# Kernel optimization log

Hardware: AMD Instinct MI355X
Metric: run time of the kernel (lower is better)

## Reference

```python
import math
import jax, jax.numpy as jnp
import numpy as np
from jax import lax

W_DIM = 512
UP = 2
K = 3
LRELU_GAIN = math.sqrt(2.0)  # bias_act def_gain for 'lrelu'
CLAMP = 256.0                # conv_clamp * gain(=1)


def setup_inputs() -> dict:
    key = jax.random.key(0)
    ks = jax.random.split(key, 8)
    B, Cin, Cout, H = 16, 512, 512, 32
    return {
        "x": jax.random.normal(ks[0], (B, Cin, H, H), jnp.float32),
        "w_latent": jax.random.normal(ks[1], (B, W_DIM), jnp.float32),
        "affine_weight": jax.random.normal(ks[2], (Cin, W_DIM), jnp.float32),
        "affine_bias": jnp.ones((Cin,), jnp.float32),  # bias_init=1
        "conv_weight": jax.random.normal(ks[3], (Cout, Cin, K, K), jnp.float32),
        "noise": jax.random.normal(ks[4], (B, 1, 2 * H, 2 * H), jnp.float32),
        "noise_strength": jax.random.uniform(ks[5], (1,), jnp.float32),
        "bias": jax.random.normal(ks[6], (Cout,), jnp.float32),
    }


def reference(x, w_latent, affine_weight, affine_bias, conv_weight, noise, noise_strength, bias):
    B, Cin, H, W = x.shape
    Cout = conv_weight.shape[0]

    # EqualFullyConnectedLayer (linear act): style = w @ (W * 1/sqrt(in)).T + b
    style = w_latent @ (affine_weight * (1.0 / math.sqrt(W_DIM))).T + affine_bias  # [B, Cin]

    # Modulate + demodulate per-sample weights: [B, Cout, Cin, K, K]
    wmod = conv_weight[None] * style[:, None, :, None, None]
    dcoefs = lax.rsqrt(jnp.sum(wmod * wmod, axis=(2, 3, 4)) + 1e-8)  # [B, Cout]
    wmod = wmod * dcoefs[:, :, None, None, None]

    # Grouped transposed conv (stride=UP), batch-as-groups trick.
    # torch.conv_transpose2d(x, w.transpose, stride=UP) == dilated conv with
    # spatially-flipped modulated weight, lhs_dilation=UP, padding=K-1.
    w_eff = wmod.reshape(B * Cout, Cin, K, K)[:, :, ::-1, ::-1]
    x1 = x.reshape(1, B * Cin, H, W)
    y = lax.conv_general_dilated(
        x1, w_eff, window_strides=(1, 1),
        padding=[(K - 1, K - 1), (K - 1, K - 1)],
        lhs_dilation=(UP, UP), feature_group_count=B,
        dimension_numbers=("NCHW", "OIHW", "NCHW"))  # [1, B*Cout, 2H+1, 2W+1]

    # upfirdn2d: FIR low-pass (1,3,3,1) outer, normalized, gain=up^2, pad (1,1,1,1)
    f1 = jnp.array([1.0, 3.0, 3.0, 1.0], jnp.float32)
    f2 = jnp.outer(f1, f1)
    f2 = f2 / f2.sum() * (UP * UP)
    yc = y.reshape(B * Cout, 1, 2 * H + 1, 2 * W + 1)
    y = lax.conv_general_dilated(
        yc, f2[None, None], window_strides=(1, 1), padding=[(1, 1), (1, 1)],
        dimension_numbers=("NCHW", "OIHW", "NCHW"))
    y = y.reshape(B, Cout, 2 * H, 2 * W)

    # noise injection + fused bias + lrelu(gain=sqrt(2)) + clamp
    y = y + noise * noise_strength[0]
    y = y + bias[None, :, None, None]
    y = jax.nn.leaky_relu(y, negative_slope=0.2) * LRELU_GAIN
    return jnp.clip(y, -CLAMP, CLAMP)
```

## Files before the change

kernel.cpp:

```cpp
#include <hip/hip_runtime.h>
#include <hip/hip_bf16.h>


typedef unsigned short u16;
typedef unsigned int u32;
typedef u16 u16x8 __attribute__((ext_vector_type(8)));
typedef __bf16 bf16x8 __attribute__((ext_vector_type(8)));
typedef float f32x4 __attribute__((ext_vector_type(4)));

#define NB 16

__device__ __forceinline__ float bf2f(u16 v) {
  unsigned int u = ((unsigned int)v) << 16;
  float f;
  __builtin_memcpy(&f, &u, 4);
  return f;
}
__device__ __forceinline__ u16 f2bf(float f) {
  __hip_bfloat16 h = __float2bfloat16(f);
  u16 r;
  __builtin_memcpy(&r, &h, 2);
  return r;
}
__device__ __forceinline__ void async16(u16* lds, const u16* g) {
  __builtin_amdgcn_global_load_lds(
      (const __attribute__((address_space(1))) u32*)g,
      (__attribute__((address_space(3))) u32*)lds, 16, 0, 0);
}

__global__ __launch_bounds__(256) void k_style(const float* __restrict__ wl,
                                               const float* __restrict__ aw,
                                               const float* __restrict__ ab,
                                               float* __restrict__ style) {
  __shared__ float lw[512];
  const int b = blockIdx.y;
  const int c = blockIdx.x * 256 + threadIdx.x;
  for (int k = threadIdx.x; k < 512; k += 256) lw[k] = wl[b * 512 + k];
  __syncthreads();
  const float* row = aw + (size_t)c * 512;
  float acc = 0.f;
#pragma unroll 8
  for (int k = 0; k < 512; ++k) acc += lw[k] * row[k];
  style[b * 512 + c] = acc * 0.04419417382415922f + ab[c];
}

__global__ __launch_bounds__(256) void k_wprep(const float* __restrict__ cw,
                                               const float* __restrict__ style,
                                               float* __restrict__ dcoef,
                                               u16* __restrict__ W2) {
  __shared__ u16 lw[4608];
  __shared__ float wsq[512];
  const int o = blockIdx.x, t = threadIdx.x;
  const float* src = cw + (size_t)o * 4608;
  for (int v = t; v < 4608; v += 256) {
    unsigned c = (unsigned)v / 9u;
    unsigned kp = (unsigned)v % 9u;
    lw[kp * 512 + c] = f2bf(src[v]);
  }
  for (int c = t; c < 512; c += 256) {
    const float* p = src + (size_t)c * 9;
    float s = 0.f;
#pragma unroll
    for (int k = 0; k < 9; ++k) {
      float v = p[k];
      s += v * v;
    }
    wsq[c] = s;
  }
  __syncthreads();
  u16* dst = W2 + (size_t)o * 4608;
  for (int v = t; v < 576; v += 256)
    *(u16x8*)(dst + v * 8) = *(const u16x8*)(lw + v * 8);
  const int w = t >> 6, l = t & 63;
  for (int b = w; b < NB; b += 4) {
    float part = 0.f;
#pragma unroll
    for (int c = l; c < 512; c += 64) {
      float st = style[b * 512 + c];
      part += st * st * wsq[c];
    }
#pragma unroll
    for (int off = 32; off; off >>= 1) part += __shfl_down(part, off, 64);
    if (l == 0) dcoef[b * 512 + o] = 1.0f / sqrtf(part + 1e-8f);
  }
}

__global__ __launch_bounds__(256) void k_xt(const float* __restrict__ x,
                                            const float* __restrict__ style,
                                            u16* __restrict__ xT) {
  __shared__ u16 tile[64 * 66];
  const int b = blockIdx.z, c0 = blockIdx.y << 6, s0 = blockIdx.x << 6;
  const int t = threadIdx.x;
#pragma unroll
  for (int i = 0; i < 16; ++i) {
    int e = i * 256 + t;
    int cc = e >> 6, ss = e & 63;
    int c = c0 + cc;
    float v = x[(size_t)(b * 512 + c) * 1024 + s0 + ss] * style[b * 512 + c];
    tile[cc * 66 + ss] = f2bf(v);
  }
  __syncthreads();
#pragma unroll
  for (int e = 0; e < 2; ++e) {
    int idx = e * 256 + t;
    int sc = idx >> 3;
    int cg = (idx & 7) << 3;
    u16x8 v;
#pragma unroll
    for (int g = 0; g < 8; ++g) v[g] = tile[(cg + g) * 66 + sc];
    *(u16x8*)(xT + (size_t)(b * 1024 + s0 + sc) * 512 + c0 + cg) = v;
  }
}

__global__ __launch_bounds__(512, 2) void k_gemm(const u16* __restrict__ W2,
                                                 const u16* __restrict__ xT,
                                                 u16* __restrict__ Z) {
  __shared__ u16 At[4][8192];
  __shared__ u16 Bt[4][8192];
  const int t = threadIdx.x;
  const int m0 = blockIdx.y << 8;
  const int n0 = blockIdx.x << 8;
  const int l = t & 63;
  const int w = t >> 6;
  const int wm = w >> 2;
  const int wn = w & 3;
  const int lrow = l & 15;
  const int lk = l >> 4;

  const int sr = t >> 2;
  const int sch = ((t & 3) + (sr >> 1)) & 3;
  const u16* gA = W2 + (size_t)(m0 + sr) * 512 + (sch << 3);
  const u16* gB = xT + (size_t)(n0 + sr) * 512 + (sch << 3);
  const int wb = w << 9;

  const int sk8 = ((lk - (lrow >> 1)) & 3) << 3;
  const int arow = (wm << 7) + lrow;
  const int brow = (wn << 6) + lrow;

  f32x4 acc[8][4] = {};

#define STAGE_A(nb_, kt_)                                   \
  async16(&At[nb_][wb], gA + (kt_) * 32);                   \
  async16(&At[nb_][4096 + wb], gA + (kt_) * 32 + 65536)
#define STAGE_B(nb_, kt_)                                   \
  async16(&Bt[nb_][wb], gB + (kt_) * 32);                   \
  async16(&Bt[nb_][4096 + wb], gB + (kt_) * 32 + 65536)

  STAGE_A(0, 0);
  STAGE_B(0, 0);
  STAGE_A(1, 1);
  STAGE_B(1, 1);
  asm volatile("s_waitcnt vmcnt(4)" ::: "memory");
  asm volatile("s_barrier" ::: "memory");

  for (int kt = 0; kt < 16; ++kt) {
    const int buf = kt & 3;
    const int nb = (kt + 2) & 3;
    const u16* Ab = At[buf];
    const u16* Bb = Bt[buf];
    bf16x8 av[4], bv[4], av2[4];

#pragma unroll
    for (int i = 0; i < 4; ++i)
      av[i] = *(const bf16x8*)(Ab + (arow + i * 16) * 32 + sk8);
#pragma unroll
    for (int j = 0; j < 4; ++j)
      bv[j] = *(const bf16x8*)(Bb + (brow + j * 16) * 32 + sk8);
    if (kt < 14) { STAGE_A(nb, kt + 2); }
    asm volatile("s_barrier" ::: "memory");
    asm volatile("s_waitcnt lgkmcnt(0)" ::: "memory");
    __builtin_amdgcn_sched_barrier(0);
    __builtin_amdgcn_s_setprio(1);
#pragma unroll
    for (int i = 0; i < 4; ++i)
#pragma unroll
      for (int j = 0; j < 4; ++j)
        acc[i][j] = __builtin_amdgcn_mfma_f32_16x16x32_bf16(av[i], bv[j], acc[i][j], 0, 0, 0);
    __builtin_amdgcn_s_setprio(0);
    asm volatile("s_barrier" ::: "memory");

#pragma unroll
    for (int i = 0; i < 4; ++i)
      av2[i] = *(const bf16x8*)(Ab + (arow + 64 + i * 16) * 32 + sk8);
    if (kt < 14) { STAGE_B(nb, kt + 2); }
    asm volatile("s_barrier" ::: "memory");
    asm volatile("s_waitcnt lgkmcnt(0)" ::: "memory");
    __builtin_amdgcn_sched_barrier(0);
    __builtin_amdgcn_s_setprio(1);
#pragma unroll
    for (int i = 0; i < 4; ++i)
#pragma unroll
      for (int j = 0; j < 4; ++j)
        acc[i + 4][j] = __builtin_amdgcn_mfma_f32_16x16x32_bf16(av2[i], bv[j], acc[i + 4][j], 0, 0, 0);
    __builtin_amdgcn_s_setprio(0);

    if (kt < 14) {
      asm volatile("s_waitcnt vmcnt(4)" ::: "memory");
    } else if (kt == 14) {
      asm volatile("s_waitcnt vmcnt(0)" ::: "memory");
    }
    asm volatile("s_barrier" ::: "memory");
  }
#undef STAGE_A
#undef STAGE_B

  const int mr = m0 + (wm << 7) + (lk << 2);
  const int nc = n0 + (wn << 6) + lrow;
#pragma unroll
  for (int i = 0; i < 8; ++i)
#pragma unroll
    for (int j = 0; j < 4; ++j)
#pragma unroll
      for (int r = 0; r < 4; ++r)
        Z[(size_t)(mr + i * 16 + r) * 16384 + nc + j * 16] = f2bf(acc[i][j][r]);
}

__global__ __launch_bounds__(256) void k_scatter(
    const u16* __restrict__ Z, const float* __restrict__ dcoef,
    const float* __restrict__ noise, const float* __restrict__ nstr,
    const float* __restrict__ bias, float* __restrict__ out) {
  __shared__ u16 Zl[9 * 1024];
  __shared__ float Hl[3 * 2048];
  const int o = blockIdx.x;
  const int b = blockIdx.y;
  const int t = threadIdx.x;
  const u16* Zp = Z + (size_t)o * 9 * 16384 + (size_t)b * 1024;
  for (int v = t; v < 1152; v += 256) {
    int kp = v >> 7, off = (v & 127) << 3;
    *(u16x8*)(Zl + kp * 1024 + off) = *(const u16x8*)(Zp + (size_t)kp * 16384 + off);
  }
  __syncthreads();
#pragma unroll
  for (int e = 0; e < 12; ++e) {
    int idx = e * 256 + t;
    int ky = idx >> 10;
    int i = (idx >> 5) & 31;
    int j = idx & 31;
    const u16* P0 = Zl + (ky * 3 + 0) * 1024 + i * 32;
    const u16* P1 = P0 + 1024;
    const u16* P2 = P0 + 2048;
    float Ej = bf2f(P0[j]) + (j >= 1 ? bf2f(P2[j - 1]) : 0.f);
    float Ej1 = (j < 31 ? bf2f(P0[j + 1]) : 0.f) + bf2f(P2[j]);
    float Ojm = j >= 1 ? bf2f(P1[j - 1]) : 0.f;
    float Oj = bf2f(P1[j]);
    float Ojp = j < 31 ? bf2f(P1[j + 1]) : 0.f;
    float* hp = Hl + ky * 2048 + i * 64 + j;
    hp[0] = Ojm + 3.f * Ej + 3.f * Oj + Ej1;
    hp[32] = Ej + 3.f * Oj + 3.f * Ej1 + Ojp;
  }
  __syncthreads();
  const float dc = dcoef[b * 512 + o] * 0.0625f;
  const float ns = nstr[0];
  const float bo = bias[o];
  const int n = t & 63;
  const int i0 = (t >> 6) << 3;
  const int sw = ((n & 1) << 5) | (n >> 1);
  const float* H0 = Hl + sw;
  const float* H1 = Hl + 2048 + sw;
  const float* H2 = Hl + 4096 + sw;
  float h0 = H0[i0 * 64];
  float h1 = H1[i0 * 64];
  float h1p = (i0 > 0) ? H1[(i0 - 1) * 64] : 0.f;
  float h2p = (i0 > 0) ? H2[(i0 - 1) * 64] : 0.f;
  const float* nz = noise + ((size_t)b << 12) + n;
  float* op = out + (((size_t)(b * 512 + o)) << 12) + n;
#pragma unroll
  for (int s = 0; s < 8; ++s) {
    int i = i0 + s;
    float h0n = (i < 31) ? H0[(i + 1) * 64] : 0.f;
    float h1n = (i < 31) ? H1[(i + 1) * 64] : 0.f;
    float h2 = H2[i * 64];
    float ev = h1p + 3.f * (h0 + h2p) + 3.f * h1 + (h0n + h2);
    float od = (h0 + h2p) + 3.f * h1 + 3.f * (h0n + h2) + h1n;
    int m = 2 * i;
    float v0 = ev * dc + nz[(size_t)m * 64] * ns + bo;
    v0 = (v0 > 0.f ? v0 : 0.2f * v0) * 1.4142135623730951f;
    v0 = fminf(fmaxf(v0, -256.f), 256.f);
    op[(size_t)m * 64] = v0;
    float v1 = od * dc + nz[(size_t)(m + 1) * 64] * ns + bo;
    v1 = (v1 > 0.f ? v1 : 0.2f * v1) * 1.4142135623730951f;
    v1 = fminf(fmaxf(v1, -256.f), 256.f);
    op[(size_t)(m + 1) * 64] = v1;
    h0 = h0n;
    h1p = h1;
    h1 = h1n;
    h2p = h2;
  }
}

extern "C" void kernel_launch(void* const* d_in, const int* in_sizes, int n_in,
                              void* d_out, int out_size, void* d_ws, size_t ws_size,
                              hipStream_t stream) {
  const float* x = (const float*)d_in[0];
  const float* wl = (const float*)d_in[1];
  const float* aw = (const float*)d_in[2];
  const float* ab = (const float*)d_in[3];
  const float* cw = (const float*)d_in[4];
  const float* noise = (const float*)d_in[5];
  const float* nstr = (const float*)d_in[6];
  const float* bias = (const float*)d_in[7];
  float* out = (float*)d_out;

  float* style = (float*)d_ws;
  float* dcoef = style + 8192;
  u16* W2 = (u16*)(dcoef + 8192);
  u16* xT = W2 + 4608 * 512;
  u16* Z = xT + (size_t)16384 * 512;

  k_style<<<dim3(2, 16), 256, 0, stream>>>(wl, aw, ab, style);
  k_wprep<<<dim3(512), 256, 0, stream>>>(cw, style, dcoef, W2);
  k_xt<<<dim3(16, 8, 16), 256, 0, stream>>>(x, style, xT);
  k_gemm<<<dim3(64, 18), 512, 0, stream>>>(W2, xT, Z);
  k_scatter<<<dim3(512, 16), 256, 0, stream>>>(Z, dcoef, noise, nstr, bias, out);
}
```

Measured before the change: 382.6 us.

## Deepen GEMM prefetch to three stages, swizzle block order, coalesce style GEMV

The GEMM's async global-to-LDS pipeline now keeps three k-tiles in flight instead of two, using all four LDS buffers, so load latency is better hidden. The vmcnt waits are adjusted to match, and the final iteration skips its barrier. Block indices are remapped in groups of eight so concurrently running blocks share A/B tiles in L2. The style GEMV now uses one wavefront per output row with float4 coalesced reads and a shuffle reduction. The cost is a more complex wait-count scheme that must match the number of loads still outstanding.

New measurement: 392.8 us. +2.7%, slower.

```diff
diff --git a/kernel.cpp b/kernel.cpp
--- a/kernel.cpp
+++ b/kernel.cpp
@@ -34,14 +34,24 @@
                                                float* __restrict__ style) {
   __shared__ float lw[512];
   const int b = blockIdx.y;
-  const int c = blockIdx.x * 256 + threadIdx.x;
-  for (int k = threadIdx.x; k < 512; k += 256) lw[k] = wl[b * 512 + k];
-  __syncthreads();
-  const float* row = aw + (size_t)c * 512;
-  float acc = 0.f;
-#pragma unroll 8
-  for (int k = 0; k < 512; ++k) acc += lw[k] * row[k];
-  style[b * 512 + c] = acc * 0.04419417382415922f + ab[c];
+  const int c0 = blockIdx.x << 6;
+  const int t = threadIdx.x;
+  for (int k = t; k < 512; k += 256) lw[k] = wl[b * 512 + k];
+  __syncthreads();
+  const int w = t >> 6, l = t & 63;
+  const float4 lv0 = *(const float4*)(lw + (l << 2));
+  const float4 lv1 = *(const float4*)(lw + 256 + (l << 2));
+  for (int r = w; r < 64; r += 4) {
+    const int c = c0 + r;
+    const float* row = aw + (size_t)c * 512 + (l << 2);
+    const float4 a0 = *(const float4*)(row);
+    const float4 a1 = *(const float4*)(row + 256);
+    float acc = lv0.x * a0.x + lv0.y * a0.y + lv0.z * a0.z + lv0.w * a0.w +
+                lv1.x * a1.x + lv1.y * a1.y + lv1.z * a1.z + lv1.w * a1.w;
+#pragma unroll
+    for (int off = 32; off; off >>= 1) acc += __shfl_down(acc, off, 64);
+    if (l == 0) style[b * 512 + c] = acc * 0.04419417382415922f + ab[c];
+  }
 }
 
 __global__ __launch_bounds__(256) void k_wprep(const float* __restrict__ cw,
@@ -118,8 +128,11 @@
   __shared__ u16 At[4][8192];
   __shared__ u16 Bt[4][8192];
   const int t = threadIdx.x;
-  const int m0 = blockIdx.y << 8;
-  const int n0 = blockIdx.x << 8;
+  const int lin = blockIdx.y * 64 + blockIdx.x;
+  const int xlog = ((lin & 7) << 3) | ((lin >> 3) & 7);
+  const int ylog = lin >> 6;
+  const int m0 = ylog << 8;
+  const int n0 = xlog << 8;
   const int l = t & 63;
   const int w = t >> 6;
   const int wm = w >> 2;
@@ -150,12 +163,14 @@
   STAGE_B(0, 0);
   STAGE_A(1, 1);
   STAGE_B(1, 1);
-  asm volatile("s_waitcnt vmcnt(4)" ::: "memory");
+  STAGE_A(2, 2);
+  STAGE_B(2, 2);
+  asm volatile("s_waitcnt vmcnt(8)" ::: "memory");
   asm volatile("s_barrier" ::: "memory");
 
   for (int kt = 0; kt < 16; ++kt) {
     const int buf = kt & 3;
-    const int nb = (kt + 2) & 3;
+    const int nb = (kt + 3) & 3;
     const u16* Ab = At[buf];
     const u16* Bb = Bt[buf];
     bf16x8 av[4], bv[4], av2[4];
@@ -166,7 +181,7 @@
 #pragma unroll
     for (int j = 0; j < 4; ++j)
       bv[j] = *(const bf16x8*)(Bb + (brow + j * 16) * 32 + sk8);
-    if (kt < 14) { STAGE_A(nb, kt + 2); }
+    if (kt < 13) { STAGE_A(nb, kt + 3); }
     asm volatile("s_barrier" ::: "memory");
     asm volatile("s_waitcnt lgkmcnt(0)" ::: "memory");
     __builtin_amdgcn_sched_barrier(0);
@@ -182,7 +197,7 @@
 #pragma unroll
     for (int i = 0; i < 4; ++i)
       av2[i] = *(const bf16x8*)(Ab + (arow + 64 + i * 16) * 32 + sk8);
-    if (kt < 14) { STAGE_B(nb, kt + 2); }
+    if (kt < 13) { STAGE_B(nb, kt + 3); }
     asm volatile("s_barrier" ::: "memory");
     asm volatile("s_waitcnt lgkmcnt(0)" ::: "memory");
     __builtin_amdgcn_sched_barrier(0);
@@ -194,12 +209,16 @@
         acc[i + 4][j] = __builtin_amdgcn_mfma_f32_16x16x32_bf16(av2[i], bv[j], acc[i + 4][j], 0, 0, 0);
     __builtin_amdgcn_s_setprio(0);
 
-    if (kt < 14) {
+    if (kt <= 12) {
+      asm volatile("s_waitcnt vmcnt(8)" ::: "memory");
+      asm volatile("s_barrier" ::: "memory");
+    } else if (kt == 13) {
       asm volatile("s_waitcnt vmcnt(4)" ::: "memory");
+      asm volatile("s_barrier" ::: "memory");
     } else if (kt == 14) {
       asm volatile("s_waitcnt vmcnt(0)" ::: "memory");
+      asm volatile("s_barrier" ::: "memory");
     }
-    asm volatile("s_barrier" ::: "memory");
   }
 #undef STAGE_A
 #undef STAGE_B
@@ -307,7 +326,7 @@
   u16* xT = W2 + 4608 * 512;
   u16* Z = xT + (size_t)16384 * 512;
 
-  k_style<<<dim3(2, 16), 256, 0, stream>>>(wl, aw, ab, style);
+  k_style<<<dim3(8, 16), 256, 0, stream>>>(wl, aw, ab, style);
   k_wprep<<<dim3(512), 256, 0, stream>>>(cw, style, dcoef, W2);
   k_xt<<<dim3(16, 8, 16), 256, 0, stream>>>(x, style, xT);
   k_gemm<<<dim3(64, 18), 512, 0, stream>>>(W2, xT, Z);
```
